# Kernel tuning notes

Hardware: AMD Instinct MI355X
Metric: run time of the kernel (lower is better)

## Reference

```python
import jax, jax.numpy as jnp
import numpy as np

B, S, H = 2, 2048, 1024
NH = 16
HD = H // NH  # 64


def _linear_params(key, fan_in, fan_out):
    k1, k2 = jax.random.split(key)
    bound = 1.0 / np.sqrt(fan_in)
    W = jax.random.uniform(k1, (fan_in, fan_out), jnp.float32, -bound, bound)
    b = jax.random.uniform(k2, (fan_out,), jnp.float32, -bound, bound)
    return W, b


def setup_inputs() -> dict:
    key = jax.random.key(0)
    ks = jax.random.split(key, 7)
    hidden_states = jax.random.normal(ks[0], (B, S, H), jnp.float32)
    governance_embeddings = jax.random.normal(ks[1], (B, H), jnp.float32)
    Wq, bq = _linear_params(ks[2], H, H)
    Wk, bk = _linear_params(ks[3], H, H)
    Wv, bv = _linear_params(ks[4], H, H)
    Wgq, bgq = _linear_params(ks[5], H, H)
    Wgk, bgk = _linear_params(ks[6], H, H)
    return {
        'hidden_states': hidden_states,
        'governance_embeddings': governance_embeddings,
        'Wq': Wq, 'bq': bq, 'Wk': Wk, 'bk': bk, 'Wv': Wv, 'bv': bv,
        'Wgq': Wgq, 'bgq': bgq, 'Wgk': Wgk, 'bgk': bgk,
    }


def reference(hidden_states, governance_embeddings, Wq, bq, Wk, bk, Wv, bv, Wgq, bgq, Wgk, bgk):
    b, s, h = hidden_states.shape
    # QKV projections -> [b, nh, s, hd]
    def heads(x):
        return x.reshape(b, s, NH, HD).transpose(0, 2, 1, 3)
    q = heads(hidden_states @ Wq + bq)
    k = heads(hidden_states @ Wk + bk)
    v = heads(hidden_states @ Wv + bv)

    scale = jnp.float32(1.0 / np.sqrt(HD))
    scores = jnp.einsum('bhid,bhjd->bhij', q, k) * scale  # [b,nh,s,s]

    # governance bias: one query per example vs per-token keys (unscaled)
    gq = (governance_embeddings @ Wgq + bgq).reshape(b, NH, HD)      # [b,nh,hd]
    gk = (hidden_states @ Wgk + bgk).reshape(b, s, NH, HD)           # [b,s,nh,hd]
    gov_scores = jnp.einsum('bhd,bshd->bhs', gq, gk)                 # [b,nh,s]

    # bias is constant along key dim (torch expand on last axis)
    combined = scores + 0.1 * gov_scores[..., :, None]

    probs = jax.nn.softmax(combined, axis=-1)  # dropout = identity (eval)
    context = jnp.einsum('bhij,bhjd->bhid', probs, v)
    context = context.transpose(0, 2, 1, 3).reshape(b, s, h)

    entropy = -jnp.sum(probs * jnp.log(probs + 1e-8), axis=-1).mean()
    influence = jnp.abs(gov_scores).mean()  # mean over expanded tensor == mean over [b,nh,s]
    concentration = probs.max(axis=-1).mean()
    return context, entropy, influence, concentration
```

## Files before the change

kernel.cpp:

```cpp
#include <hip/hip_runtime.h>


typedef unsigned short u16;
typedef __attribute__((ext_vector_type(8))) short bf16x8;
typedef __attribute__((ext_vector_type(4))) float f32x4;
typedef __attribute__((ext_vector_type(4))) u16 u16x4;
typedef __attribute__((ext_vector_type(4))) float float4v;

typedef const __attribute__((address_space(1))) void gvoid_t;
typedef __attribute__((address_space(3))) void lvoid_t;

__device__ __forceinline__ void gl_lds16(const void* g, void* l) {
  __builtin_amdgcn_global_load_lds((gvoid_t*)g, (lvoid_t*)l, 16, 0, 0);
}

__device__ __forceinline__ u16 f2bf(float x) {
  union { float f; unsigned u; } v; v.f = x;
  unsigned r = v.u + 0x7fffu + ((v.u >> 16) & 1u);
  return (u16)(r >> 16);
}
__device__ __forceinline__ float bf2f(u16 h) {
  union { unsigned u; float f; } v; v.u = ((unsigned)h) << 16; return v.f;
}
__device__ __forceinline__ unsigned pk2(float hi, float lo) {
  union { float f; unsigned u; } a, b; a.f = hi; b.f = lo;
  return __builtin_amdgcn_perm(a.u, b.u, 0x07060302u);
}


__global__ void conv_hs(const float* __restrict__ in, u16* __restrict__ out) {
  int i = blockIdx.x * 256 + threadIdx.x;
  const float4v* in4 = (const float4v*)in;
  float4v a = in4[i * 2], b = in4[i * 2 + 1];
  bf16x8 v;
  v[0] = (short)f2bf(a.x); v[1] = (short)f2bf(a.y);
  v[2] = (short)f2bf(a.z); v[3] = (short)f2bf(a.w);
  v[4] = (short)f2bf(b.x); v[5] = (short)f2bf(b.y);
  v[6] = (short)f2bf(b.z); v[7] = (short)f2bf(b.w);
  *(bf16x8*)&out[(size_t)i * 8] = v;
}

__global__ void conv_w(const float* __restrict__ W0, const float* __restrict__ W1,
                       const float* __restrict__ W2, const float* __restrict__ W3,
                       u16* __restrict__ WB) {
  __shared__ __align__(16) u16 T[64][72];
  int mat = blockIdx.y;
  const float* W = (mat == 0) ? W0 : (mat == 1) ? W1 : (mat == 2) ? W2 : W3;
  int k0 = (blockIdx.x >> 4) * 64, n0 = (blockIdx.x & 15) * 64;
  int tx = threadIdx.x;
#pragma unroll
  for (int p = 0; p < 4; ++p) {
    int chunk = p * 256 + tx;
    int row = chunk >> 4, cp = chunk & 15;
    float4v v = *(const float4v*)&W[(size_t)(k0 + row) * 1024 + n0 + cp * 4];
    u16x4 o; o.x = f2bf(v.x); o.y = f2bf(v.y); o.z = f2bf(v.z); o.w = f2bf(v.w);
    *(u16x4*)&T[row][cp * 4] = o;
  }
  __syncthreads();
#pragma unroll
  for (int p = 0; p < 2; ++p) {
    int chunk = p * 256 + tx;
    int nrow = chunk >> 3, cp = chunk & 7;
    bf16x8 v;
#pragma unroll
    for (int e = 0; e < 8; ++e) v[e] = (short)T[cp * 8 + e][nrow];
    *(bf16x8*)&WB[(size_t)(mat * 1024 + n0 + nrow) * 1024 + k0 + cp * 8] = v;
  }
}

__global__ __launch_bounds__(256, 2) void gemm_qkvg(
    const u16* __restrict__ A, const u16* __restrict__ Bw,
    const float* __restrict__ bq, const float* __restrict__ bk,
    const float* __restrict__ bv, const float* __restrict__ bgk,
    u16* __restrict__ Qb, u16* __restrict__ Kb,
    u16* __restrict__ Vb, u16* __restrict__ GKb) {
  __shared__ __align__(16) u16 As[128 * 32];
  __shared__ __align__(16) u16 Bs[128 * 32];
  const int tid = threadIdx.x, lane = tid & 63, wv = tid >> 6;
  const int li = lane & 15, quad = lane >> 4;
  const int bid = blockIdx.x;
  const int nb = bid & 31, mb = bid >> 5;
  const u16* Ap = A + (size_t)(mb * 128) * 1024;
  const u16* Bp = Bw + (size_t)(nb * 128) * 1024;
  const int wm0 = (wv >> 1) * 64, wn0 = (wv & 1) * 64;

  f32x4 acc[4][4];
#pragma unroll
  for (int t = 0; t < 4; ++t)
#pragma unroll
    for (int u = 0; u < 4; ++u) acc[t][u] = (f32x4){0.f, 0.f, 0.f, 0.f};

  for (int kt = 0; kt < 32; ++kt) {
    __syncthreads();
#pragma unroll
    for (int jj = 0; jj < 2; ++jj) {
      int j = wv * 2 + jj;
      int row = j * 16 + (lane >> 2);
      int co = lane & 3;
      gl_lds16(Ap + (size_t)row * 1024 + kt * 32 + co * 8, &As[j * 512]);
      gl_lds16(Bp + (size_t)row * 1024 + kt * 32 + co * 8, &Bs[j * 512]);
    }
    __syncthreads();
    bf16x8 af[4], bf[4];
#pragma unroll
    for (int t = 0; t < 4; ++t)
      af[t] = *(const bf16x8*)&As[(wm0 + t * 16 + li) * 32 + quad * 8];
#pragma unroll
    for (int u = 0; u < 4; ++u)
      bf[u] = *(const bf16x8*)&Bs[(wn0 + u * 16 + li) * 32 + quad * 8];
#pragma unroll
    for (int t = 0; t < 4; ++t)
#pragma unroll
      for (int u = 0; u < 4; ++u)
        acc[t][u] = __builtin_amdgcn_mfma_f32_16x16x32_bf16(af[t], bf[u], acc[t][u], 0, 0, 0);
  }

  const int nbase = nb * 128;
  const int mat = nbase >> 10;
  const float* bias = (mat == 0) ? bq : (mat == 1) ? bk : (mat == 2) ? bv : bgk;
  u16* outp = (mat == 0) ? Qb : (mat == 1) ? Kb : (mat == 2) ? Vb : GKb;
  const float qscale = (mat == 0) ? 0.125f : 1.0f;
#pragma unroll
  for (int t = 0; t < 4; ++t)
#pragma unroll
    for (int u = 0; u < 4; ++u) {
      int col = (nbase & 1023) + wn0 + u * 16 + li;
      float bb = bias[col];
#pragma unroll
      for (int r = 0; r < 4; ++r) {
        int row = mb * 128 + wm0 + t * 16 + quad * 4 + r;
        outp[(size_t)row * 1024 + col] = f2bf((acc[t][u][r] + bb) * qscale);
      }
    }
}

__global__ void transpose_v(const u16* __restrict__ Vb, u16* __restrict__ Vt) {
  __shared__ __align__(16) u16 T[64][72];
  int s0 = blockIdx.x * 64, d0 = blockIdx.y * 64, b = blockIdx.z;
  const u16* inp = Vb + (size_t)b * 2048 * 1024;
  u16* outp = Vt + (size_t)b * 1024 * 2048;
  int tx = threadIdx.x;
#pragma unroll
  for (int p = 0; p < 2; ++p) {
    int chunk = p * 256 + tx;
    int row = chunk >> 3, cp = chunk & 7;
    *(bf16x8*)&T[row][cp * 8] =
        *(const bf16x8*)&inp[(size_t)(s0 + row) * 1024 + d0 + cp * 8];
  }
  __syncthreads();
#pragma unroll
  for (int p = 0; p < 2; ++p) {
    int chunk = p * 256 + tx;
    int drow = chunk >> 3, cp = chunk & 7;
    bf16x8 v;
#pragma unroll
    for (int e = 0; e < 8; ++e) v[e] = (short)T[cp * 8 + e][drow];
    *(bf16x8*)&outp[(size_t)(d0 + drow) * 2048 + s0 + cp * 8] = v;
  }
}

__global__ void gq_init(const float* __restrict__ bgq, float* __restrict__ gq) {
  int t = blockIdx.x * 256 + threadIdx.x;
  gq[t] = bgq[t & 1023];
}
__global__ void gq_partial(const float* __restrict__ ge, const float* __restrict__ Wgq,
                           float* __restrict__ gq) {
  int kb = blockIdx.x, b = blockIdx.y;
  int col0 = threadIdx.x * 4;
  float4v s = {0.f, 0.f, 0.f, 0.f};
  for (int k = kb * 32; k < kb * 32 + 32; ++k) {
    float g = ge[b * 1024 + k];
    float4v w = *(const float4v*)&Wgq[(size_t)k * 1024 + col0];
    s.x += g * w.x; s.y += g * w.y; s.z += g * w.z; s.w += g * w.w;
  }
  float* o = &gq[b * 1024 + col0];
  atomicAdd(&o[0], s.x); atomicAdd(&o[1], s.y);
  atomicAdd(&o[2], s.z); atomicAdd(&o[3], s.w);
}

__global__ __launch_bounds__(256, 2) void attn_kernel(
    const u16* __restrict__ Qb, const u16* __restrict__ Kb,
    const u16* __restrict__ Vt, float* __restrict__ out,
    float* __restrict__ acc ) {
  __shared__ __align__(16) u16 Ks[128 * 64];
  __shared__ __align__(16) u16 Vs[64 * 128];
  __shared__ __align__(16) u16 Ps[4][16 * 40];
  __shared__ float redE[4], redC[4];

  const int tid = threadIdx.x, lane = tid & 63, wv = tid >> 6;
  const int li = lane & 15, quad = lane >> 4;
  const int bx = blockIdx.x;
  const int bh = bx & 31, qb = bx >> 5;
  const int b = bh >> 4, h = bh & 15;
  const int wq0 = wv * 32;

  const u16* Qp = Qb + (size_t)(b * 2048 + qb * 128 + wq0) * 1024 + h * 64;
  const u16* Kp = Kb + (size_t)(b * 2048) * 1024 + h * 64;
  const u16* Vp = Vt + (size_t)b * (1024 * 2048) + (size_t)(h * 64) * 2048;

  bf16x8 qf[2][2];
#pragma unroll
  for (int t = 0; t < 2; ++t)
#pragma unroll
    for (int kc = 0; kc < 2; ++kc)
      qf[t][kc] = *(const bf16x8*)&Qp[(size_t)(t * 16 + li) * 1024 + kc * 32 + quad * 8];

  float m_st[2], l_st[2], e_st[2];
  f32x4 accO[4][2];
#pragma unroll
  for (int t = 0; t < 2; ++t) { m_st[t] = -3.0e38f; l_st[t] = 0.f; e_st[t] = 0.f; }
#pragma unroll
  for (int mt = 0; mt < 4; ++mt)
#pragma unroll
    for (int t = 0; t < 2; ++t) accO[mt][t] = (f32x4){0.f, 0.f, 0.f, 0.f};

  for (int kt = 0; kt < 16; ++kt) {
    __syncthreads();
    const u16* Kpt = Kp + (size_t)(kt * 128) * 1024;
#pragma unroll
    for (int jj = 0; jj < 4; ++jj) {
      int j = wv * 4 + jj;
      int row = j * 8 + (lane >> 3);
      int c16 = (lane & 7) ^ (row & 7);
      gl_lds16(Kpt + (size_t)row * 1024 + c16 * 8, &Ks[j * 512]);
    }
#pragma unroll
    for (int jj = 0; jj < 4; ++jj) {
      int j = wv * 4 + jj;
      int row = j * 4 + (lane >> 4);
      int c16 = (lane & 15) ^ (row & 7);
      gl_lds16(Vp + (size_t)row * 2048 + kt * 128 + c16 * 8, &Vs[j * 512]);
    }
    __syncthreads();

    f32x4 S[8][2];
#pragma unroll
    for (int u = 0; u < 8; ++u) {
      int row = u * 16 + li;
      bf16x8 a0 = *(const bf16x8*)&Ks[row * 64 + ((quad) ^ (li & 7)) * 8];
      bf16x8 a1 = *(const bf16x8*)&Ks[row * 64 + ((4 + quad) ^ (li & 7)) * 8];
#pragma unroll
      for (int t = 0; t < 2; ++t) {
        f32x4 c = {0.f, 0.f, 0.f, 0.f};
        c = __builtin_amdgcn_mfma_f32_16x16x32_bf16(a0, qf[t][0], c, 0, 0, 0);
        c = __builtin_amdgcn_mfma_f32_16x16x32_bf16(a1, qf[t][1], c, 0, 0, 0);
        S[u][t] = c;
      }
    }

    float alpha_[2];
#pragma unroll
    for (int t = 0; t < 2; ++t) {
      float cm = S[0][t][0];
#pragma unroll
      for (int u = 0; u < 8; ++u)
#pragma unroll
        for (int r = 0; r < 4; ++r) cm = fmaxf(cm, S[u][t][r]);
      cm = fmaxf(cm, __shfl_xor(cm, 16, 64));
      cm = fmaxf(cm, __shfl_xor(cm, 32, 64));
      float mo = m_st[t], mn = fmaxf(mo, cm);
      m_st[t] = mn;
      float al = __expf(mo - mn);
      alpha_[t] = al;
      float ps = 0.f, es = 0.f;
#pragma unroll
      for (int u = 0; u < 8; ++u)
#pragma unroll
        for (int r = 0; r < 4; ++r) {
          float s = S[u][t][r];
          float p = __expf(s - mn);
          ps += p;
          es = __builtin_fmaf(p, s, es);
          S[u][t][r] = p;
        }
      l_st[t] = l_st[t] * al + ps;
      e_st[t] = e_st[t] * al + es;
    }
#pragma unroll
    for (int mt = 0; mt < 4; ++mt)
#pragma unroll
      for (int t = 0; t < 2; ++t) {
        accO[mt][t][0] *= alpha_[t]; accO[mt][t][1] *= alpha_[t];
        accO[mt][t][2] *= alpha_[t]; accO[mt][t][3] *= alpha_[t];
      }

    u16* Pw = &Ps[wv][0];
#pragma unroll
    for (int c = 0; c < 4; ++c) {
      bf16x8 av[4];
#pragma unroll
      for (int mt = 0; mt < 4; ++mt) {
        int row = mt * 16 + li;
        av[mt] = *(const bf16x8*)&Vs[row * 128 + ((c * 4 + quad) ^ (li & 7)) * 8];
      }
#pragma unroll
      for (int t = 0; t < 2; ++t) {
        uint2 w0, w1;
        w0.x = pk2(S[2 * c][t][1], S[2 * c][t][0]);
        w0.y = pk2(S[2 * c][t][3], S[2 * c][t][2]);
        w1.x = pk2(S[2 * c + 1][t][1], S[2 * c + 1][t][0]);
        w1.y = pk2(S[2 * c + 1][t][3], S[2 * c + 1][t][2]);
        *(uint2*)&Pw[li * 40 + quad * 4] = w0;
        *(uint2*)&Pw[li * 40 + 16 + quad * 4] = w1;
        bf16x8 bp = *(const bf16x8*)&Pw[li * 40 + quad * 8];
#pragma unroll
        for (int mt = 0; mt < 4; ++mt)
          accO[mt][t] = __builtin_amdgcn_mfma_f32_16x16x32_bf16(av[mt], bp, accO[mt][t], 0, 0, 0);
      }
    }
  }

  float* outp = out + (size_t)(b * 2048 + qb * 128 + wq0) * 1024 + h * 64;
  float entw = 0.f, concw = 0.f;
#pragma unroll
  for (int t = 0; t < 2; ++t) {
    float lsum = l_st[t];
    lsum += __shfl_xor(lsum, 16, 64); lsum += __shfl_xor(lsum, 32, 64);
    float esum = e_st[t];
    esum += __shfl_xor(esum, 16, 64); esum += __shfl_xor(esum, 32, 64);
    float inv = 1.0f / lsum;
    entw += m_st[t] + __logf(lsum) - esum * inv;
    concw += inv;
#pragma unroll
    for (int mt = 0; mt < 4; ++mt) {
      f32x4 o = accO[mt][t];
      o[0] *= inv; o[1] *= inv; o[2] *= inv; o[3] *= inv;
      *(float4v*)&outp[(size_t)(t * 16 + li) * 1024 + mt * 16 + quad * 4] = *(float4v*)&o;
    }
  }
#pragma unroll
  for (int off = 1; off < 64; off <<= 1) {
    entw += __shfl_xor(entw, off, 64);
    concw += __shfl_xor(concw, off, 64);
  }
  if (lane == 0) { redE[wv] = entw * 0.25f; redC[wv] = concw * 0.25f; }
  __syncthreads();
  if (tid == 0) {
    atomicAdd(&acc[0], redE[0] + redE[1] + redE[2] + redE[3]);
    atomicAdd(&acc[1], redC[0] + redC[1] + redC[2] + redC[3]);
  }
}

__global__ void gov_kernel(const u16* __restrict__ GKb, const float* __restrict__ gq,
                           float* __restrict__ acc_inf) {
  __shared__ float redI[4];
  int lane = threadIdx.x & 63, wv = threadIdx.x >> 6;
  int wid = blockIdx.x * 4 + wv;
  int b = wid >> 11, s = wid & 2047;
  const u16* gk = GKb + (size_t)(b * 2048 + s) * 1024 + lane * 16;
  const float* gqp = gq + b * 1024 + lane * 16;
  bf16x8 g0 = *(const bf16x8*)gk, g1 = *(const bf16x8*)(gk + 8);
  float4v q0 = *(const float4v*)&gqp[0], q1 = *(const float4v*)&gqp[4];
  float4v q2 = *(const float4v*)&gqp[8], q3 = *(const float4v*)&gqp[12];
  float sum = 0.f;
  sum += bf2f((u16)g0[0]) * q0.x + bf2f((u16)g0[1]) * q0.y +
         bf2f((u16)g0[2]) * q0.z + bf2f((u16)g0[3]) * q0.w;
  sum += bf2f((u16)g0[4]) * q1.x + bf2f((u16)g0[5]) * q1.y +
         bf2f((u16)g0[6]) * q1.z + bf2f((u16)g0[7]) * q1.w;
  sum += bf2f((u16)g1[0]) * q2.x + bf2f((u16)g1[1]) * q2.y +
         bf2f((u16)g1[2]) * q2.z + bf2f((u16)g1[3]) * q2.w;
  sum += bf2f((u16)g1[4]) * q3.x + bf2f((u16)g1[5]) * q3.y +
         bf2f((u16)g1[6]) * q3.z + bf2f((u16)g1[7]) * q3.w;
  sum += __shfl_xor(sum, 1, 64);
  sum += __shfl_xor(sum, 2, 64);
  float v = ((lane & 3) == 0) ? fabsf(sum) : 0.f;
  v += __shfl_xor(v, 4, 64);
  v += __shfl_xor(v, 8, 64);
  v += __shfl_xor(v, 16, 64);
  v += __shfl_xor(v, 32, 64);
  if (lane == 0) redI[wv] = v;
  __syncthreads();
  if (threadIdx.x == 0)
    atomicAdd(acc_inf, redI[0] + redI[1] + redI[2] + redI[3]);
}

__global__ void finalize(const float* __restrict__ acc, float* __restrict__ out) {
  if (threadIdx.x == 0) {
    out[0] = acc[0] * (1.f / 65536.f);
    out[1] = acc[2] * (1.f / 65536.f);
    out[2] = acc[1] * (1.f / 65536.f);
  }
}

extern "C" void kernel_launch(void* const* d_in, const int* in_sizes, int n_in,
                              void* d_out, int out_size, void* d_ws, size_t ws_size,
                              hipStream_t stream) {
  (void)in_sizes; (void)n_in; (void)out_size; (void)ws_size;
  const float* hs  = (const float*)d_in[0];
  const float* ge  = (const float*)d_in[1];
  const float* Wq  = (const float*)d_in[2];
  const float* bq  = (const float*)d_in[3];
  const float* Wk  = (const float*)d_in[4];
  const float* bk  = (const float*)d_in[5];
  const float* Wv  = (const float*)d_in[6];
  const float* bv  = (const float*)d_in[7];
  const float* Wgq = (const float*)d_in[8];
  const float* bgq = (const float*)d_in[9];
  const float* Wgk = (const float*)d_in[10];
  const float* bgk = (const float*)d_in[11];

  char* ws = (char*)d_ws;
  u16* hsB = (u16*)(ws);
  u16* WB  = (u16*)(ws + (size_t)(8 << 20));
  u16* Qb  = (u16*)(ws + (size_t)(16 << 20));
  u16* Kb  = (u16*)(ws + (size_t)(24 << 20));
  u16* Vb  = (u16*)(ws + (size_t)(32 << 20));
  u16* GKb = (u16*)(ws + (size_t)(40 << 20));
  u16* Vt  = (u16*)(ws + (size_t)(48 << 20));
  float* gq  = (float*)(ws + (size_t)(56 << 20));
  float* acc = (float*)(ws + (size_t)(56 << 20) + 16384);
  float* out = (float*)d_out;

  hipMemsetAsync(acc, 0, 3 * sizeof(float), stream);
  conv_hs<<<2048, 256, 0, stream>>>(hs, hsB);
  conv_w<<<dim3(256, 4), 256, 0, stream>>>(Wq, Wk, Wv, Wgk, WB);
  gq_init<<<8, 256, 0, stream>>>(bgq, gq);
  gemm_qkvg<<<1024, 256, 0, stream>>>(hsB, WB, bq, bk, bv, bgk, Qb, Kb, Vb, GKb);
  transpose_v<<<dim3(32, 16, 2), 256, 0, stream>>>(Vb, Vt);
  gq_partial<<<dim3(32, 2), 256, 0, stream>>>(ge, Wgq, gq);
  attn_kernel<<<512, 256, 0, stream>>>(Qb, Kb, Vt, out, acc);
  gov_kernel<<<1024, 256, 0, stream>>>(GKb, gq, acc + 2);
  finalize<<<1, 64, 0, stream>>>(acc, out + 4194304);
}
```

Measured before the change: 241.2 us.

## Fuse prep kernels, write V transposed from GEMM, drop online softmax rescale

After: 254.9 us. 1.06x slower.

```diff
diff --git a/kernel.cpp b/kernel.cpp
--- a/kernel.cpp
+++ b/kernel.cpp
@@ -4,7 +4,6 @@
 typedef unsigned short u16;
 typedef __attribute__((ext_vector_type(8))) short bf16x8;
 typedef __attribute__((ext_vector_type(4))) float f32x4;
-typedef __attribute__((ext_vector_type(4))) u16 u16x4;
 typedef __attribute__((ext_vector_type(4))) float float4v;
 
 typedef const __attribute__((address_space(1))) void gvoid_t;
@@ -27,53 +26,77 @@
   return __builtin_amdgcn_perm(a.u, b.u, 0x07060302u);
 }
 
-
-__global__ void conv_hs(const float* __restrict__ in, u16* __restrict__ out) {
-  int i = blockIdx.x * 256 + threadIdx.x;
-  const float4v* in4 = (const float4v*)in;
-  float4v a = in4[i * 2], b = in4[i * 2 + 1];
-  bf16x8 v;
-  v[0] = (short)f2bf(a.x); v[1] = (short)f2bf(a.y);
-  v[2] = (short)f2bf(a.z); v[3] = (short)f2bf(a.w);
-  v[4] = (short)f2bf(b.x); v[5] = (short)f2bf(b.y);
-  v[6] = (short)f2bf(b.z); v[7] = (short)f2bf(b.w);
-  *(bf16x8*)&out[(size_t)i * 8] = v;
-}
-
-__global__ void conv_w(const float* __restrict__ W0, const float* __restrict__ W1,
-                       const float* __restrict__ W2, const float* __restrict__ W3,
-                       u16* __restrict__ WB) {
-  __shared__ __align__(16) u16 T[64][72];
-  int mat = blockIdx.y;
-  const float* W = (mat == 0) ? W0 : (mat == 1) ? W1 : (mat == 2) ? W2 : W3;
-  int k0 = (blockIdx.x >> 4) * 64, n0 = (blockIdx.x & 15) * 64;
-  int tx = threadIdx.x;
-#pragma unroll
-  for (int p = 0; p < 4; ++p) {
-    int chunk = p * 256 + tx;
-    int row = chunk >> 4, cp = chunk & 15;
-    float4v v = *(const float4v*)&W[(size_t)(k0 + row) * 1024 + n0 + cp * 4];
-    u16x4 o; o.x = f2bf(v.x); o.y = f2bf(v.y); o.z = f2bf(v.z); o.w = f2bf(v.w);
-    *(u16x4*)&T[row][cp * 4] = o;
-  }
-  __syncthreads();
-#pragma unroll
-  for (int p = 0; p < 2; ++p) {
-    int chunk = p * 256 + tx;
-    int nrow = chunk >> 3, cp = chunk & 7;
+__global__ void prep(const float* __restrict__ hs,
+                     const float* __restrict__ W0, const float* __restrict__ W1,
+                     const float* __restrict__ W2, const float* __restrict__ W3,
+                     const float* __restrict__ ge, const float* __restrict__ Wgq,
+                     u16* __restrict__ hsB, u16* __restrict__ WB,
+                     float* __restrict__ gq_part) {
+  int bx = blockIdx.x, tid = threadIdx.x;
+  if (bx < 2048) {
+    int i = bx * 256 + tid;
+    const float4v* in4 = (const float4v*)hs;
+    float4v a = in4[i * 2], b = in4[i * 2 + 1];
     bf16x8 v;
-#pragma unroll
-    for (int e = 0; e < 8; ++e) v[e] = (short)T[cp * 8 + e][nrow];
-    *(bf16x8*)&WB[(size_t)(mat * 1024 + n0 + nrow) * 1024 + k0 + cp * 8] = v;
-  }
-}
-
-__global__ __launch_bounds__(256, 2) void gemm_qkvg(
+    v[0] = (short)f2bf(a.x); v[1] = (short)f2bf(a.y);
+    v[2] = (short)f2bf(a.z); v[3] = (short)f2bf(a.w);
+    v[4] = (short)f2bf(b.x); v[5] = (short)f2bf(b.y);
+    v[6] = (short)f2bf(b.z); v[7] = (short)f2bf(b.w);
+    *(bf16x8*)&hsB[(size_t)i * 8] = v;
+    return;
+  }
+  if (bx < 2560) {
+    int idx = bx - 2048;
+    int kb = idx & 127, mat = idx >> 7;
+    const float* W = (mat == 0) ? W0 : (mat == 1) ? W1 : (mat == 2) ? W2 : W3;
+    int n0 = tid * 4;
+    float4v r[8];
+#pragma unroll
+    for (int j = 0; j < 8; ++j)
+      r[j] = *(const float4v*)&W[(size_t)(kb * 8 + j) * 1024 + n0];
+#pragma unroll
+    for (int c = 0; c < 4; ++c) {
+      uint4 o;
+      o.x = pk2(r[1][c], r[0][c]); o.y = pk2(r[3][c], r[2][c]);
+      o.z = pk2(r[5][c], r[4][c]); o.w = pk2(r[7][c], r[6][c]);
+      *(uint4*)&WB[(size_t)(mat * 1024 + n0 + c) * 1024 + kb * 8] = o;
+    }
+    return;
+  }
+  {
+    int idx = bx - 2560;
+    int kb = idx >> 1, b = idx & 1;
+    int col0 = tid * 4;
+    float4v s = {0.f, 0.f, 0.f, 0.f};
+    for (int k = kb * 32; k < kb * 32 + 32; ++k) {
+      float g = ge[b * 1024 + k];
+      float4v w = *(const float4v*)&Wgq[(size_t)k * 1024 + col0];
+      s.x += g * w.x; s.y += g * w.y; s.z += g * w.z; s.w += g * w.w;
+    }
+    *(float4v*)&gq_part[(size_t)idx * 1024 + col0] = s;
+  }
+}
+
+__global__ __launch_bounds__(256, 3) void gemm_qkvg(
     const u16* __restrict__ A, const u16* __restrict__ Bw,
     const float* __restrict__ bq, const float* __restrict__ bk,
     const float* __restrict__ bv, const float* __restrict__ bgk,
+    const float* __restrict__ bgq, const float* __restrict__ gq_part,
     u16* __restrict__ Qb, u16* __restrict__ Kb,
-    u16* __restrict__ Vb, u16* __restrict__ GKb) {
+    u16* __restrict__ GKb, u16* __restrict__ Vt,
+    float* __restrict__ gq_final, float* __restrict__ acc3) {
+  if (blockIdx.x == 1024) {
+    int tid = threadIdx.x;
+    if (tid < 3) acc3[tid] = 0.f;
+#pragma unroll
+    for (int i = 0; i < 8; ++i) {
+      int t = tid + i * 256;
+      float s = bgq[t & 1023];
+      for (int kb = 0; kb < 32; ++kb) s += gq_part[(size_t)(kb * 2 + (t >> 10)) * 1024 + (t & 1023)];
+      gq_final[t] = s;
+    }
+    return;
+  }
   __shared__ __align__(16) u16 As[128 * 32];
   __shared__ __align__(16) u16 Bs[128 * 32];
   const int tid = threadIdx.x, lane = tid & 63, wv = tid >> 6;
@@ -117,78 +140,80 @@
 
   const int nbase = nb * 128;
   const int mat = nbase >> 10;
-  const float* bias = (mat == 0) ? bq : (mat == 1) ? bk : (mat == 2) ? bv : bgk;
-  u16* outp = (mat == 0) ? Qb : (mat == 1) ? Kb : (mat == 2) ? Vb : GKb;
-  const float qscale = (mat == 0) ? 0.125f : 1.0f;
-#pragma unroll
-  for (int t = 0; t < 4; ++t)
-#pragma unroll
-    for (int u = 0; u < 4; ++u) {
-      int col = (nbase & 1023) + wn0 + u * 16 + li;
-      float bb = bias[col];
-#pragma unroll
-      for (int r = 0; r < 4; ++r) {
-        int row = mb * 128 + wm0 + t * 16 + quad * 4 + r;
-        outp[(size_t)row * 1024 + col] = f2bf((acc[t][u][r] + bb) * qscale);
-      }
-    }
-}
-
-__global__ void transpose_v(const u16* __restrict__ Vb, u16* __restrict__ Vt) {
-  __shared__ __align__(16) u16 T[64][72];
-  int s0 = blockIdx.x * 64, d0 = blockIdx.y * 64, b = blockIdx.z;
-  const u16* inp = Vb + (size_t)b * 2048 * 1024;
-  u16* outp = Vt + (size_t)b * 1024 * 2048;
-  int tx = threadIdx.x;
-#pragma unroll
-  for (int p = 0; p < 2; ++p) {
-    int chunk = p * 256 + tx;
-    int row = chunk >> 3, cp = chunk & 7;
-    *(bf16x8*)&T[row][cp * 8] =
-        *(const bf16x8*)&inp[(size_t)(s0 + row) * 1024 + d0 + cp * 8];
-  }
-  __syncthreads();
-#pragma unroll
-  for (int p = 0; p < 2; ++p) {
-    int chunk = p * 256 + tx;
-    int drow = chunk >> 3, cp = chunk & 7;
-    bf16x8 v;
-#pragma unroll
-    for (int e = 0; e < 8; ++e) v[e] = (short)T[cp * 8 + e][drow];
-    *(bf16x8*)&outp[(size_t)(d0 + drow) * 2048 + s0 + cp * 8] = v;
-  }
-}
-
-__global__ void gq_init(const float* __restrict__ bgq, float* __restrict__ gq) {
-  int t = blockIdx.x * 256 + threadIdx.x;
-  gq[t] = bgq[t & 1023];
-}
-__global__ void gq_partial(const float* __restrict__ ge, const float* __restrict__ Wgq,
-                           float* __restrict__ gq) {
-  int kb = blockIdx.x, b = blockIdx.y;
-  int col0 = threadIdx.x * 4;
-  float4v s = {0.f, 0.f, 0.f, 0.f};
-  for (int k = kb * 32; k < kb * 32 + 32; ++k) {
-    float g = ge[b * 1024 + k];
-    float4v w = *(const float4v*)&Wgq[(size_t)k * 1024 + col0];
-    s.x += g * w.x; s.y += g * w.y; s.z += g * w.z; s.w += g * w.w;
-  }
-  float* o = &gq[b * 1024 + col0];
-  atomicAdd(&o[0], s.x); atomicAdd(&o[1], s.y);
-  atomicAdd(&o[2], s.z); atomicAdd(&o[3], s.w);
-}
-
-__global__ __launch_bounds__(256, 2) void attn_kernel(
+  if (mat == 2) {
+#pragma unroll
+    for (int t = 0; t < 4; ++t)
+#pragma unroll
+      for (int u = 0; u < 4; ++u) {
+        int col = (nbase & 1023) + wn0 + u * 16 + li;
+        float bb = bv[col];
+        int row = mb * 128 + wm0 + t * 16 + quad * 4;
+        int b = row >> 11, s = row & 2047;
+        uint2 w;
+        w.x = pk2(acc[t][u][1] + bb, acc[t][u][0] + bb);
+        w.y = pk2(acc[t][u][3] + bb, acc[t][u][2] + bb);
+        *(uint2*)&Vt[(size_t)b * (1024 * 2048) + (size_t)col * 2048 + s] = w;
+      }
+  } else {
+    const float* bias = (mat == 0) ? bq : (mat == 1) ? bk : bgk;
+    u16* outp = (mat == 0) ? Qb : (mat == 1) ? Kb : GKb;
+    const float qscale = (mat == 0) ? 0.18033688f : 1.0f;
+#pragma unroll
+    for (int t = 0; t < 4; ++t)
+#pragma unroll
+      for (int u = 0; u < 4; ++u) {
+        int col = (nbase & 1023) + wn0 + u * 16 + li;
+        float bb = bias[col];
+#pragma unroll
+        for (int r = 0; r < 4; ++r) {
+          int row = mb * 128 + wm0 + t * 16 + quad * 4 + r;
+          outp[(size_t)row * 1024 + col] = f2bf((acc[t][u][r] + bb) * qscale);
+        }
+      }
+  }
+}
+
+__global__ __launch_bounds__(256, 2) void attn_gov(
     const u16* __restrict__ Qb, const u16* __restrict__ Kb,
-    const u16* __restrict__ Vt, float* __restrict__ out,
-    float* __restrict__ acc ) {
-  __shared__ __align__(16) u16 Ks[128 * 64];
-  __shared__ __align__(16) u16 Vs[64 * 128];
-  __shared__ __align__(16) u16 Ps[4][16 * 40];
-  __shared__ float redE[4], redC[4];
+    const u16* __restrict__ Vt, const u16* __restrict__ GKb,
+    const float* __restrict__ gq_final, float* __restrict__ out,
+    float* __restrict__ acc3 ) {
+  __shared__ __align__(16) u16 Ks[2][128 * 64];
+  __shared__ __align__(16) u16 Vs[2][64 * 128];
+  __shared__ __align__(16) u16 Ps[4][16 * 36];
+  __shared__ float red[8];
 
   const int tid = threadIdx.x, lane = tid & 63, wv = tid >> 6;
   const int li = lane & 15, quad = lane >> 4;
+
+  if (blockIdx.x >= 512) {
+    int wid = (blockIdx.x - 512) * 4 + wv;
+    int b = wid >> 11, s = wid & 2047;
+    const u16* gk = GKb + (size_t)(b * 2048 + s) * 1024 + lane * 16;
+    const float* gqp = gq_final + b * 1024 + lane * 16;
+    bf16x8 g0 = *(const bf16x8*)gk, g1 = *(const bf16x8*)(gk + 8);
+    float4v q0 = *(const float4v*)&gqp[0], q1 = *(const float4v*)&gqp[4];
+    float4v q2 = *(const float4v*)&gqp[8], q3 = *(const float4v*)&gqp[12];
+    float sum = 0.f;
+    sum += bf2f((u16)g0[0]) * q0.x + bf2f((u16)g0[1]) * q0.y +
+           bf2f((u16)g0[2]) * q0.z + bf2f((u16)g0[3]) * q0.w;
+    sum += bf2f((u16)g0[4]) * q1.x + bf2f((u16)g0[5]) * q1.y +
+           bf2f((u16)g0[6]) * q1.z + bf2f((u16)g0[7]) * q1.w;
+    sum += bf2f((u16)g1[0]) * q2.x + bf2f((u16)g1[1]) * q2.y +
+           bf2f((u16)g1[2]) * q2.z + bf2f((u16)g1[3]) * q2.w;
+    sum += bf2f((u16)g1[4]) * q3.x + bf2f((u16)g1[5]) * q3.y +
+           bf2f((u16)g1[6]) * q3.z + bf2f((u16)g1[7]) * q3.w;
+    sum += __shfl_xor(sum, 1, 64);
+    sum += __shfl_xor(sum, 2, 64);
+    float v = ((lane & 3) == 0) ? fabsf(sum) : 0.f;
+    v += __shfl_xor(v, 4, 64);  v += __shfl_xor(v, 8, 64);
+    v += __shfl_xor(v, 16, 64); v += __shfl_xor(v, 32, 64);
+    if (lane == 0) red[wv] = v;
+    __syncthreads();
+    if (tid == 0) atomicAdd(&acc3[2], red[0] + red[1] + red[2] + red[3]);
+    return;
+  }
+
   const int bx = blockIdx.x;
   const int bh = bx & 31, qb = bx >> 5;
   const int b = bh >> 4, h = bh & 15;
@@ -214,31 +239,50 @@
 #pragma unroll
     for (int t = 0; t < 2; ++t) accO[mt][t] = (f32x4){0.f, 0.f, 0.f, 0.f};
 
+#pragma unroll
+  for (int jj = 0; jj < 4; ++jj) {
+    int j = wv * 4 + jj;
+    int row = j * 8 + (lane >> 3);
+    int c16 = (lane & 7) ^ (row & 7);
+    gl_lds16(Kp + (size_t)row * 1024 + c16 * 8, &Ks[0][j * 512]);
+  }
+#pragma unroll
+  for (int jj = 0; jj < 4; ++jj) {
+    int j = wv * 4 + jj;
+    int row = j * 4 + (lane >> 4);
+    int c16 = (lane & 15) ^ (row & 7);
+    gl_lds16(Vp + (size_t)row * 2048 + c16 * 8, &Vs[0][j * 512]);
+  }
+
   for (int kt = 0; kt < 16; ++kt) {
+    const int cur = kt & 1;
     __syncthreads();
-    const u16* Kpt = Kp + (size_t)(kt * 128) * 1024;
-#pragma unroll
-    for (int jj = 0; jj < 4; ++jj) {
-      int j = wv * 4 + jj;
-      int row = j * 8 + (lane >> 3);
-      int c16 = (lane & 7) ^ (row & 7);
-      gl_lds16(Kpt + (size_t)row * 1024 + c16 * 8, &Ks[j * 512]);
-    }
-#pragma unroll
-    for (int jj = 0; jj < 4; ++jj) {
-      int j = wv * 4 + jj;
-      int row = j * 4 + (lane >> 4);
-      int c16 = (lane & 15) ^ (row & 7);
-      gl_lds16(Vp + (size_t)row * 2048 + kt * 128 + c16 * 8, &Vs[j * 512]);
-    }
-    __syncthreads();
+    if (kt < 15) {
+      const u16* Kpt = Kp + (size_t)((kt + 1) * 128) * 1024;
+#pragma unroll
+      for (int jj = 0; jj < 4; ++jj) {
+        int j = wv * 4 + jj;
+        int row = j * 8 + (lane >> 3);
+        int c16 = (lane & 7) ^ (row & 7);
+        gl_lds16(Kpt + (size_t)row * 1024 + c16 * 8, &Ks[cur ^ 1][j * 512]);
+      }
+#pragma unroll
+      for (int jj = 0; jj < 4; ++jj) {
+        int j = wv * 4 + jj;
+        int row = j * 4 + (lane >> 4);
+        int c16 = (lane & 15) ^ (row & 7);
+        gl_lds16(Vp + (size_t)row * 2048 + (kt + 1) * 128 + c16 * 8, &Vs[cur ^ 1][j * 512]);
+      }
+    }
+    const u16* KsC = &Ks[cur][0];
+    const u16* VsC = &Vs[cur][0];
 
     f32x4 S[8][2];
 #pragma unroll
     for (int u = 0; u < 8; ++u) {
       int row = u * 16 + li;
-      bf16x8 a0 = *(const bf16x8*)&Ks[row * 64 + ((quad) ^ (li & 7)) * 8];
-      bf16x8 a1 = *(const bf16x8*)&Ks[row * 64 + ((4 + quad) ^ (li & 7)) * 8];
+      bf16x8 a0 = *(const bf16x8*)&KsC[row * 64 + ((quad) ^ (li & 7)) * 8];
+      bf16x8 a1 = *(const bf16x8*)&KsC[row * 64 + ((4 + quad) ^ (li & 7)) * 8];
 #pragma unroll
       for (int t = 0; t < 2; ++t) {
         f32x4 c = {0.f, 0.f, 0.f, 0.f};
@@ -248,41 +292,24 @@
       }
     }
 
-    float alpha_[2];
 #pragma unroll
     for (int t = 0; t < 2; ++t) {
-      float cm = S[0][t][0];
-#pragma unroll
-      for (int u = 0; u < 8; ++u)
-#pragma unroll
-        for (int r = 0; r < 4; ++r) cm = fmaxf(cm, S[u][t][r]);
-      cm = fmaxf(cm, __shfl_xor(cm, 16, 64));
-      cm = fmaxf(cm, __shfl_xor(cm, 32, 64));
-      float mo = m_st[t], mn = fmaxf(mo, cm);
-      m_st[t] = mn;
-      float al = __expf(mo - mn);
-      alpha_[t] = al;
-      float ps = 0.f, es = 0.f;
+      float cmx = m_st[t], ps = 0.f, es = 0.f;
 #pragma unroll
       for (int u = 0; u < 8; ++u)
 #pragma unroll
         for (int r = 0; r < 4; ++r) {
           float s = S[u][t][r];
-          float p = __expf(s - mn);
+          cmx = fmaxf(cmx, s);
+          float p = exp2f(s);
           ps += p;
           es = __builtin_fmaf(p, s, es);
           S[u][t][r] = p;
         }
-      l_st[t] = l_st[t] * al + ps;
-      e_st[t] = e_st[t] * al + es;
-    }
-#pragma unroll
-    for (int mt = 0; mt < 4; ++mt)
-#pragma unroll
-      for (int t = 0; t < 2; ++t) {
-        accO[mt][t][0] *= alpha_[t]; accO[mt][t][1] *= alpha_[t];
-        accO[mt][t][2] *= alpha_[t]; accO[mt][t][3] *= alpha_[t];
-      }
+      m_st[t] = cmx;
+      l_st[t] += ps;
+      e_st[t] += es;
+    }
 
     u16* Pw = &Ps[wv][0];
 #pragma unroll
@@ -291,7 +318,7 @@
 #pragma unroll
       for (int mt = 0; mt < 4; ++mt) {
         int row = mt * 16 + li;
-        av[mt] = *(const bf16x8*)&Vs[row * 128 + ((c * 4 + quad) ^ (li & 7)) * 8];
+        av[mt] = *(const bf16x8*)&VsC[row * 128 + ((c * 4 + quad) ^ (li & 7)) * 8];
       }
 #pragma unroll
       for (int t = 0; t < 2; ++t) {
@@ -300,9 +327,9 @@
         w0.y = pk2(S[2 * c][t][3], S[2 * c][t][2]);
         w1.x = pk2(S[2 * c + 1][t][1], S[2 * c + 1][t][0]);
         w1.y = pk2(S[2 * c + 1][t][3], S[2 * c + 1][t][2]);
-        *(uint2*)&Pw[li * 40 + quad * 4] = w0;
-        *(uint2*)&Pw[li * 40 + 16 + quad * 4] = w1;
-        bf16x8 bp = *(const bf16x8*)&Pw[li * 40 + quad * 8];
+        *(uint2*)&Pw[li * 36 + quad * 4] = w0;
+        *(uint2*)&Pw[li * 36 + 16 + quad * 4] = w1;
+        bf16x8 bp = *(const bf16x8*)&Pw[li * 36 + quad * 8];
 #pragma unroll
         for (int mt = 0; mt < 4; ++mt)
           accO[mt][t] = __builtin_amdgcn_mfma_f32_16x16x32_bf16(av[mt], bp, accO[mt][t], 0, 0, 0);
@@ -318,9 +345,11 @@
     lsum += __shfl_xor(lsum, 16, 64); lsum += __shfl_xor(lsum, 32, 64);
     float esum = e_st[t];
     esum += __shfl_xor(esum, 16, 64); esum += __shfl_xor(esum, 32, 64);
+    float mm = m_st[t];
+    mm = fmaxf(mm, __shfl_xor(mm, 16, 64)); mm = fmaxf(mm, __shfl_xor(mm, 32, 64));
     float inv = 1.0f / lsum;
-    entw += m_st[t] + __logf(lsum) - esum * inv;
-    concw += inv;
+    entw += __logf(lsum) - 0.69314718f * esum * inv;
+    concw += exp2f(mm) * inv;
 #pragma unroll
     for (int mt = 0; mt < 4; ++mt) {
       f32x4 o = accO[mt][t];
@@ -333,52 +362,19 @@
     entw += __shfl_xor(entw, off, 64);
     concw += __shfl_xor(concw, off, 64);
   }
-  if (lane == 0) { redE[wv] = entw * 0.25f; redC[wv] = concw * 0.25f; }
+  if (lane == 0) { red[wv] = entw * 0.25f; red[4 + wv] = concw * 0.25f; }
   __syncthreads();
   if (tid == 0) {
-    atomicAdd(&acc[0], redE[0] + redE[1] + redE[2] + redE[3]);
-    atomicAdd(&acc[1], redC[0] + redC[1] + redC[2] + redC[3]);
-  }
-}
-
-__global__ void gov_kernel(const u16* __restrict__ GKb, const float* __restrict__ gq,
-                           float* __restrict__ acc_inf) {
-  __shared__ float redI[4];
-  int lane = threadIdx.x & 63, wv = threadIdx.x >> 6;
-  int wid = blockIdx.x * 4 + wv;
-  int b = wid >> 11, s = wid & 2047;
-  const u16* gk = GKb + (size_t)(b * 2048 + s) * 1024 + lane * 16;
-  const float* gqp = gq + b * 1024 + lane * 16;
-  bf16x8 g0 = *(const bf16x8*)gk, g1 = *(const bf16x8*)(gk + 8);
-  float4v q0 = *(const float4v*)&gqp[0], q1 = *(const float4v*)&gqp[4];
-  float4v q2 = *(const float4v*)&gqp[8], q3 = *(const float4v*)&gqp[12];
-  float sum = 0.f;
-  sum += bf2f((u16)g0[0]) * q0.x + bf2f((u16)g0[1]) * q0.y +
-         bf2f((u16)g0[2]) * q0.z + bf2f((u16)g0[3]) * q0.w;
-  sum += bf2f((u16)g0[4]) * q1.x + bf2f((u16)g0[5]) * q1.y +
-         bf2f((u16)g0[6]) * q1.z + bf2f((u16)g0[7]) * q1.w;
-  sum += bf2f((u16)g1[0]) * q2.x + bf2f((u16)g1[1]) * q2.y +
-         bf2f((u16)g1[2]) * q2.z + bf2f((u16)g1[3]) * q2.w;
-  sum += bf2f((u16)g1[4]) * q3.x + bf2f((u16)g1[5]) * q3.y +
-         bf2f((u16)g1[6]) * q3.z + bf2f((u16)g1[7]) * q3.w;
-  sum += __shfl_xor(sum, 1, 64);
-  sum += __shfl_xor(sum, 2, 64);
-  float v = ((lane & 3) == 0) ? fabsf(sum) : 0.f;
-  v += __shfl_xor(v, 4, 64);
-  v += __shfl_xor(v, 8, 64);
-  v += __shfl_xor(v, 16, 64);
-  v += __shfl_xor(v, 32, 64);
-  if (lane == 0) redI[wv] = v;
-  __syncthreads();
-  if (threadIdx.x == 0)
-    atomicAdd(acc_inf, redI[0] + redI[1] + redI[2] + redI[3]);
-}
-
-__global__ void finalize(const float* __restrict__ acc, float* __restrict__ out) {
+    atomicAdd(&acc3[0], red[0] + red[1] + red[2] + red[3]);
+    atomicAdd(&acc3[1], red[4] + red[5] + red[6] + red[7]);
+  }
+}
+
+__global__ void finalize(const float* __restrict__ acc3, float* __restrict__ out) {
   if (threadIdx.x == 0) {
-    out[0] = acc[0] * (1.f / 65536.f);
-    out[1] = acc[2] * (1.f / 65536.f);
-    out[2] = acc[1] * (1.f / 65536.f);
+    out[0] = acc3[0] * (1.f / 65536.f);
+    out[1] = acc3[2] * (1.f / 65536.f);
+    out[2] = acc3[1] * (1.f / 65536.f);
   }
 }
 
@@ -404,21 +400,16 @@
   u16* WB  = (u16*)(ws + (size_t)(8 << 20));
   u16* Qb  = (u16*)(ws + (size_t)(16 << 20));
   u16* Kb  = (u16*)(ws + (size_t)(24 << 20));
-  u16* Vb  = (u16*)(ws + (size_t)(32 << 20));
+  u16* Vt  = (u16*)(ws + (size_t)(32 << 20));
   u16* GKb = (u16*)(ws + (size_t)(40 << 20));
-  u16* Vt  = (u16*)(ws + (size_t)(48 << 20));
-  float* gq  = (float*)(ws + (size_t)(56 << 20));
-  float* acc = (float*)(ws + (size_t)(56 << 20) + 16384);
+  float* gq_part  = (float*)(ws + (size_t)(48 << 20));
+  float* gq_final = (float*)(ws + (size_t)(48 << 20) + 262144);
+  float* acc3     = (float*)(ws + (size_t)(48 << 20) + 524288);
   float* out = (float*)d_out;
 
-  hipMemsetAsync(acc, 0, 3 * sizeof(float), stream);
-  conv_hs<<<2048, 256, 0, stream>>>(hs, hsB);
-  conv_w<<<dim3(256, 4), 256, 0, stream>>>(Wq, Wk, Wv, Wgk, WB);
-  gq_init<<<8, 256, 0, stream>>>(bgq, gq);
-  gemm_qkvg<<<1024, 256, 0, stream>>>(hsB, WB, bq, bk, bv, bgk, Qb, Kb, Vb, GKb);
-  transpose_v<<<dim3(32, 16, 2), 256, 0, stream>>>(Vb, Vt);
-  gq_partial<<<dim3(32, 2), 256, 0, stream>>>(ge, Wgq, gq);
-  attn_kernel<<<512, 256, 0, stream>>>(Qb, Kb, Vt, out, acc);
-  gov_kernel<<<1024, 256, 0, stream>>>(GKb, gq, acc + 2);
-  finalize<<<1, 64, 0, stream>>>(acc, out + 4194304);
-}
+  prep<<<2624, 256, 0, stream>>>(hs, Wq, Wk, Wv, Wgk, ge, Wgq, hsB, WB, gq_part);
+  gemm_qkvg<<<1025, 256, 0, stream>>>(hsB, WB, bq, bk, bv, bgk, bgq, gq_part,
+                                      Qb, Kb, GKb, Vt, gq_final, acc3);
+  attn_gov<<<1536, 256, 0, stream>>>(Qb, Kb, Vt, GKb, gq_final, out, acc3);
+  finalize<<<1, 64, 0, stream>>>(acc3, out + 4194304);
+}
```
